# Kernel tuning notes

Measured on AMD Instinct MI355X. Metric: run time of the kernel, lower is better.

## Reference

```python
import jax, jax.numpy as jnp
import numpy as np

N = 50000      # n_nodes
S = 16         # neighbors per node
D_IN = 256     # raw feature dim
PREP = 128     # prep_len
H = 2          # n_head
OUT = 64       # per-head spec output_dim (concat_node doubles it)
MP = 2         # n_mp (metapaths)
IN2 = 2 * OUT * H  # layer-2 input dim = 256


def setup_inputs() -> dict:
    key = jax.random.key(0)
    ks = jax.random.split(key, 7)
    feats = jax.random.normal(ks[0], (N, D_IN), jnp.float32)
    prep_W = jax.random.normal(ks[1], (D_IN, PREP), jnp.float32) * 0.05
    Wx1 = jax.random.normal(ks[2], (MP, H, PREP, OUT), jnp.float32) * 0.05
    Wn1 = jax.random.normal(ks[3], (MP, H, PREP, OUT), jnp.float32) * 0.05
    Wx2 = jax.random.normal(ks[4], (MP, H, IN2, OUT), jnp.float32) * 0.05
    Wn2 = jax.random.normal(ks[5], (MP, H, IN2, OUT), jnp.float32) * 0.05
    node_neigh = jax.random.randint(ks[6], (MP, N, S), 0, N, dtype=jnp.int32)
    return {"feats": feats, "prep_W": prep_W, "Wx1": Wx1, "Wn1": Wn1,
            "Wx2": Wx2, "Wn2": Wn2, "node_neigh": node_neigh}


def _agg_layer(x, neigh, Wx, Wn):
    # x: [N, d]; neigh: [N, S]; Wx, Wn: [H, d, OUT]
    # neighbor gather + mean (the chunk_edge = all_feats[node_neigh] path)
    agg = jnp.mean(x[neigh], axis=1)                  # [N, d]
    xh = jnp.einsum('nd,hdo->nho', x, Wx)             # [N, H, OUT]
    nh = jnp.einsum('nd,hdo->nho', agg, Wn)           # [N, H, OUT]
    h = jax.nn.relu(jnp.concatenate([xh, nh], -1))    # per-head concat_node
    return h.reshape(x.shape[0], -1)                  # heads concatenated


def reference(feats, prep_W, Wx1, Wn1, Wx2, Wn2, node_neigh):
    # feats[all_ids].detach() in the original -> stop_gradient
    feats = jax.lax.stop_gradient(feats)
    outs = []
    for mp in range(MP):
        h0 = feats @ prep_W                           # prep (dummy == layer-1 prep here)
        neigh = node_neigh[mp]
        h1 = _agg_layer(h0, neigh, Wx1[mp], Wn1[mp])  # [N, 256]
        h2 = _agg_layer(h1, neigh, Wx2[mp], Wn2[mp])  # [N, 256]
        outs.append(jnp.concatenate([h1, h2], axis=-1))  # skip-buffer concat
    return jnp.stack(outs, axis=0)                    # [MP, N, 512]
```

## Files before the change

### kernel.cpp

```cpp
#include <hip/hip_runtime.h>

#define NN 50000
#define SNEI 16
#define GB 782

typedef unsigned short ushort_t;
typedef unsigned int uint_t;
typedef unsigned long long u64;
typedef __attribute__((ext_vector_type(8))) short bhalf8;
typedef __attribute__((ext_vector_type(4))) float facc4;

__device__ __forceinline__ float b2f(uint_t u) {
    union { uint_t u; float f; } x; x.u = u << 16; return x.f;
}
__device__ __forceinline__ ushort_t f2b(float f) {
    union { float f; uint_t u; } x; x.f = f;
    return (ushort_t)((x.u + 0x7FFFu + ((x.u >> 16) & 1u)) >> 16);
}
__device__ __forceinline__ u64 pack4(float a, float b, float c, float d) {
    return (u64)f2b(a) | ((u64)f2b(b) << 16) | ((u64)f2b(c) << 32) | ((u64)f2b(d) << 48);
}

typedef const __attribute__((address_space(1))) void cglb_t;
typedef __attribute__((address_space(3))) void lds3_t;
__device__ __forceinline__ void gload16(const void* g, void* l) {
    __builtin_amdgcn_global_load_lds((cglb_t*)g, (lds3_t*)l, 16, 0, 0);
}

__global__ void permSetup(const float* __restrict__ prepW,
                          const float* __restrict__ Wx1, const float* __restrict__ Wn1,
                          const float* __restrict__ Wx2, const float* __restrict__ Wn2,
                          ushort_t* __restrict__ dst)
{
    int e = blockIdx.x * 256 + threadIdx.x;
    int q8 = e >> 3, j = e & 7;
    int layer = q8 >> 14;
    int qq = q8 & 16383;
    int mp = qq >> 13, isN = (qq >> 12) & 1, q = qq & 4095;
    int lane = q & 63, nf = (q >> 6) & 7, ks = q >> 9;
    int c = nf * 16 + (lane & 15);
    int k = ks * 32 + ((lane >> 4) << 3) + j;
    float v;
    if (layer == 0) {
        const float* W1 = (isN ? Wn1 : Wx1) + mp * 16384 + (c >> 6) * 8192 + (c & 63);
        const float* pw = prepW + (size_t)k * 128;
        float s0 = 0.f, s1 = 0.f;
#pragma unroll 4
        for (int p = 0; p < 128; p += 2) {
            s0 += pw[p]     * W1[(size_t)p * 64];
            s1 += pw[p + 1] * W1[(size_t)(p + 1) * 64];
        }
        v = s0 + s1;
    } else {
        const float* W2 = (isN ? Wn2 : Wx2) + mp * 32768 + (c >> 6) * 16384 + (size_t)k * 64 + (c & 63);
        v = *W2;
    }
    dst[(size_t)q8 * 8 + j] = f2b(v);
}

template<bool XF32, bool L1>
__global__ __launch_bounds__(256, 4)
void proj_gemm(const void* __restrict__ Xv, size_t xStr,
               const ushort_t* __restrict__ W, size_t wStr,
               float* __restrict__ out, size_t oStr,
               ushort_t* __restrict__ h1, size_t hStr,
               ushort_t* __restrict__ P, size_t PStr)
{
    __shared__ bhalf8 lds[2560];
    u64* l64 = (u64*)lds;
    const int tid = threadIdx.x;
    const int lane = tid & 63;
    const int wid = tid >> 6;
    const int wave_m = wid >> 1, wave_n = wid & 1;
    const int m0 = blockIdx.x * 64;
    const int mp = blockIdx.y;

    const ushort_t* wx = W + (size_t)mp * wStr;
    const ushort_t* wn = wx + 4096 * 8;
    const float*    Xf = (const float*)Xv    + (size_t)mp * xStr;
    const ushort_t* Xb = (const ushort_t*)Xv + (size_t)mp * xStr;
    float* outp = out + (size_t)mp * oStr;
    ushort_t* h1p = L1 ? (h1 + (size_t)mp * hStr) : nullptr;
    ushort_t* Pp  = P + (size_t)mp * PStr;

    facc4 acc[2][8];
    const facc4 z = {0.f, 0.f, 0.f, 0.f};
#pragma unroll
    for (int i = 0; i < 2; ++i)
#pragma unroll
        for (int j = 0; j < 8; ++j) acc[i][j] = z;

    for (int kt = 0; kt < 4; ++kt) {
        if constexpr (XF32) {
#pragma unroll
            for (int it = 0; it < 2; ++it) {
                int s = tid + it * 256;
                int fp = s >> 6, ls = s & 63;
                int mf = fp & 3, ksl = fp >> 2;
                int grow = m0 + mf * 16 + (ls & 15); if (grow > NN - 1) grow = NN - 1;
                const float* gp = Xf + (size_t)grow * 256 + kt * 64 + ksl * 32 + ((ls >> 4) << 3);
                float4 f0 = *(const float4*)gp, f1 = *(const float4*)(gp + 4);
                l64[s * 2]     = pack4(f0.x, f0.y, f0.z, f0.w);
                l64[s * 2 + 1] = pack4(f1.x, f1.y, f1.z, f1.w);
            }
        } else {
#pragma unroll
            for (int it = 0; it < 2; ++it) {
                int u = wid + it * 4;
                int mf = u & 3, ksl = u >> 2;
                int grow = m0 + mf * 16 + (lane & 15); if (grow > NN - 1) grow = NN - 1;
                const ushort_t* src = Xb + (size_t)grow * 256 + kt * 64 + ksl * 32 + ((lane >> 4) << 3);
                gload16(src, (char*)lds + (u * 64 + lane) * 16);
            }
        }
#pragma unroll
        for (int it = 0; it < 4; ++it) {
            int cb = (it * 4 + wid) * 64;
            gload16(wx + ((size_t)kt * 1024 + cb + lane) * 8,
                    (char*)lds + (512 + cb + lane) * 16);
            gload16(wn + ((size_t)kt * 1024 + cb + lane) * 8,
                    (char*)lds + (1536 + cb + lane) * 16);
        }
        __syncthreads();
        const int wB = wave_n ? 1536 : 512;
#pragma unroll
        for (int ksl = 0; ksl < 2; ++ksl) {
            bhalf8 a0 = lds[(ksl * 4 + wave_m * 2 + 0) * 64 + lane];
            bhalf8 a1 = lds[(ksl * 4 + wave_m * 2 + 1) * 64 + lane];
#pragma unroll
            for (int nf = 0; nf < 8; ++nf) {
                bhalf8 b = lds[wB + (ksl * 8 + nf) * 64 + lane];
                acc[0][nf] = __builtin_amdgcn_mfma_f32_16x16x32_bf16(a0, b, acc[0][nf], 0, 0, 0);
                acc[1][nf] = __builtin_amdgcn_mfma_f32_16x16x32_bf16(a1, b, acc[1][nf], 0, 0, 0);
            }
        }
        __syncthreads();
    }
    const int cl = lane & 15, rg = lane >> 4;
    const int obase = L1 ? 0 : 256;
#pragma unroll
    for (int mf2 = 0; mf2 < 2; ++mf2) {
        int rowb = m0 + (wave_m * 2 + mf2) * 16 + rg * 4;
#pragma unroll
        for (int nf = 0; nf < 8; ++nf) {
            int cpr = nf * 16 + cl;
            int icol = (cpr >> 6) * 128 + (cpr & 63);
            facc4 v = acc[mf2][nf];
#pragma unroll
            for (int rr = 0; rr < 4; ++rr) {
                int row = rowb + rr;
                if (row < NN) {
                    if (wave_n == 0) {
                        float f = fmaxf(v[rr], 0.0f);
                        outp[(size_t)row * 512 + obase + icol] = f;
                        if constexpr (L1)
                            h1p[(size_t)row * 256 + icol] = f2b(f);
                    } else {
                        Pp[(size_t)(cpr >> 5) * (NN * 32) + (size_t)row * 32 + (cpr & 31)] = f2b(v[rr]);
                    }
                }
            }
        }
    }
}

template<bool L1>
__global__ __launch_bounds__(256)
void gatherS(const ushort_t* __restrict__ P, size_t PStr,
             const int* __restrict__ nb, size_t nStr,
             float* __restrict__ out, size_t oStr,
             ushort_t* __restrict__ h1, size_t hStr)
{
    const int slice = blockIdx.y;
    const int mp = blockIdx.z;
    const ushort_t* Pp = P + (size_t)mp * PStr + (size_t)slice * (NN * 32);
    const int* nbp = nb + (size_t)mp * nStr;
    float* outp = out + (size_t)mp * oStr;

    __shared__ int nls[1024];
    const int nodeBase = blockIdx.x * 64;
    {
        int i4 = nodeBase * 4 + threadIdx.x;
        int mx = NN * 4 - 1;
        if (i4 > mx) i4 = mx;
        ((int4*)nls)[threadIdx.x] = ((const int4*)nbp)[i4];
    }
    __syncthreads();

    const int nl = threadIdx.x >> 2, q = threadIdx.x & 3;
    const int node = nodeBase + nl;
    if (node >= NN) return;
    const int* nr = nls + nl * SNEI;
    float a0=0.f,a1=0.f,a2=0.f,a3=0.f,a4=0.f,a5=0.f,a6=0.f,a7=0.f;
#pragma unroll
    for (int s = 0; s < SNEI; ++s) {
        uint4 v = *(const uint4*)(Pp + (size_t)nr[s] * 32 + q * 8);
        a0 += b2f(v.x & 0xFFFFu); a1 += b2f(v.x >> 16);
        a2 += b2f(v.y & 0xFFFFu); a3 += b2f(v.y >> 16);
        a4 += b2f(v.z & 0xFFFFu); a5 += b2f(v.z >> 16);
        a6 += b2f(v.w & 0xFFFFu); a7 += b2f(v.w >> 16);
    }
    const float M = 0.0625f;
    float r0 = fmaxf(a0*M, 0.f), r1 = fmaxf(a1*M, 0.f);
    float r2 = fmaxf(a2*M, 0.f), r3 = fmaxf(a3*M, 0.f);
    float r4 = fmaxf(a4*M, 0.f), r5 = fmaxf(a5*M, 0.f);
    float r6 = fmaxf(a6*M, 0.f), r7 = fmaxf(a7*M, 0.f);
    const int head = slice >> 1;
    const int coff = head * 128 + 64 + (slice & 1) * 32 + q * 8;
    const int obase = L1 ? 0 : 256;
    float* o = outp + (size_t)node * 512 + obase + coff;
    *(float4*)o       = make_float4(r0, r1, r2, r3);
    *(float4*)(o + 4) = make_float4(r4, r5, r6, r7);
    if constexpr (L1) {
        ushort_t* hp = h1 + (size_t)mp * hStr + (size_t)node * 256 + coff;
        *(u64*)hp       = pack4(r0, r1, r2, r3);
        *(u64*)(hp + 4) = pack4(r4, r5, r6, r7);
    }
}

extern "C" void kernel_launch(void* const* d_in, const int* in_sizes, int n_in,
                              void* d_out, int out_size, void* d_ws, size_t ws_size,
                              hipStream_t stream)
{
    const float* feats  = (const float*)d_in[0];
    const float* prepWp = (const float*)d_in[1];
    const float* Wx1    = (const float*)d_in[2];
    const float* Wn1    = (const float*)d_in[3];
    const float* Wx2    = (const float*)d_in[4];
    const float* Wn2    = (const float*)d_in[5];
    const int*   neigh  = (const int*)d_in[6];
    float* out = (float*)d_out;
    ushort_t* ws = (ushort_t*)d_ws;

    const size_t permElems = 262144;
    const size_t needBatched = permElems * 2
        + 2 * ((size_t)NN * 128 * 2 + (size_t)NN * 256 * 2);
    const bool batched = ws_size >= needBatched;
    const int nmp = batched ? 2 : 1;

    ushort_t* perm = ws;
    ushort_t* P    = ws + permElems;
    ushort_t* h1   = P + (size_t)nmp * NN * 128;

    permSetup<<<1024, 256, 0, stream>>>(prepWp, Wx1, Wn1, Wx2, Wn2, perm);

    const size_t PStr = batched ? (size_t)NN * 128 : 0;
    const size_t hStr = batched ? (size_t)NN * 256 : 0;
    const size_t oStr = batched ? (size_t)NN * 512 : 0;
    const size_t nStr = batched ? (size_t)NN * SNEI : 0;
    const size_t wStr = batched ? (size_t)8192 * 8 : 0;
    const int passes = batched ? 1 : 2;

    for (int p = 0; p < passes; ++p) {
        const ushort_t* w1 = perm + (size_t)p * 8192 * 8;
        const ushort_t* w2 = perm + (size_t)(16384 + p * 8192) * 8;
        float* outp = out + (size_t)p * NN * 512;
        const int* nbp = neigh + (size_t)p * NN * SNEI;
        dim3 gp(GB, nmp), gg(GB, 4, nmp);

        proj_gemm<true, true><<<gp, 256, 0, stream>>>(
            feats, 0, w1, wStr, outp, oStr, h1, hStr, P, PStr);
        gatherS<true><<<gg, 256, 0, stream>>>(
            P, PStr, nbp, nStr, outp, oStr, h1, hStr);
        proj_gemm<false, false><<<gp, 256, 0, stream>>>(
            h1, hStr, w2, wStr, outp, oStr, nullptr, 0, P, PStr);
        gatherS<false><<<gg, 256, 0, stream>>>(
            P, PStr, nbp, nStr, outp, oStr, nullptr, 0);
    }
}
```

Before: 195.1 us.

## Drop bf16 h1 buffer, read layer-2 input from fp32 output, reorder gather grid

Removes the separate bf16 copy of h1. The layer-2 GEMM now reads the fp32 layer-1 half of the output tensor directly, converting it to bf16 while staging into LDS, which saves one buffer write. Output and P stores become nontemporal. The gather grid is flattened so that all slices and metapaths of a node block are adjacent, which should improve locality of the neighbor-index loads. In exchange, layer 2 reads 4-byte instead of 2-byte activations through a strided fp32 path rather than direct global-to-LDS loads, and the nontemporal hint may push P out of cache right before the gather kernel reads it.

```diff
diff --git a/kernel.cpp b/kernel.cpp
--- a/kernel.cpp
+++ b/kernel.cpp
@@ -9,6 +9,7 @@
 typedef unsigned long long u64;
 typedef __attribute__((ext_vector_type(8))) short bhalf8;
 typedef __attribute__((ext_vector_type(4))) float facc4;
+typedef __attribute__((ext_vector_type(4))) float f32x4;
 
 __device__ __forceinline__ float b2f(uint_t u) {
     union { uint_t u; float f; } x; x.u = u << 16; return x.f;
@@ -58,13 +59,11 @@
     dst[(size_t)q8 * 8 + j] = f2b(v);
 }
 
-template<bool XF32, bool L1>
 __global__ __launch_bounds__(256, 4)
-void proj_gemm(const void* __restrict__ Xv, size_t xStr,
-               const ushort_t* __restrict__ W, size_t wStr,
-               float* __restrict__ out, size_t oStr,
-               ushort_t* __restrict__ h1, size_t hStr,
-               ushort_t* __restrict__ P, size_t PStr)
+void proj_gemm(const float* __restrict__ X, int xPitch, size_t xMpStr,
+               const ushort_t* __restrict__ W, size_t wMpStr,
+               float* __restrict__ out, size_t oMpStr, int obase,
+               ushort_t* __restrict__ P, size_t PMpStr)
 {
     __shared__ bhalf8 lds[2560];
     u64* l64 = (u64*)lds;
@@ -75,13 +74,11 @@
     const int m0 = blockIdx.x * 64;
     const int mp = blockIdx.y;
 
-    const ushort_t* wx = W + (size_t)mp * wStr;
+    const float* Xp = X + (size_t)mp * xMpStr;
+    const ushort_t* wx = W + (size_t)mp * wMpStr;
     const ushort_t* wn = wx + 4096 * 8;
-    const float*    Xf = (const float*)Xv    + (size_t)mp * xStr;
-    const ushort_t* Xb = (const ushort_t*)Xv + (size_t)mp * xStr;
-    float* outp = out + (size_t)mp * oStr;
-    ushort_t* h1p = L1 ? (h1 + (size_t)mp * hStr) : nullptr;
-    ushort_t* Pp  = P + (size_t)mp * PStr;
+    float* outp = out + (size_t)mp * oMpStr;
+    ushort_t* Pp = P + (size_t)mp * PMpStr;
 
     facc4 acc[2][8];
     const facc4 z = {0.f, 0.f, 0.f, 0.f};
@@ -91,27 +88,16 @@
         for (int j = 0; j < 8; ++j) acc[i][j] = z;
 
     for (int kt = 0; kt < 4; ++kt) {
-        if constexpr (XF32) {
-#pragma unroll
-            for (int it = 0; it < 2; ++it) {
-                int s = tid + it * 256;
-                int fp = s >> 6, ls = s & 63;
-                int mf = fp & 3, ksl = fp >> 2;
-                int grow = m0 + mf * 16 + (ls & 15); if (grow > NN - 1) grow = NN - 1;
-                const float* gp = Xf + (size_t)grow * 256 + kt * 64 + ksl * 32 + ((ls >> 4) << 3);
-                float4 f0 = *(const float4*)gp, f1 = *(const float4*)(gp + 4);
-                l64[s * 2]     = pack4(f0.x, f0.y, f0.z, f0.w);
-                l64[s * 2 + 1] = pack4(f1.x, f1.y, f1.z, f1.w);
-            }
-        } else {
-#pragma unroll
-            for (int it = 0; it < 2; ++it) {
-                int u = wid + it * 4;
-                int mf = u & 3, ksl = u >> 2;
-                int grow = m0 + mf * 16 + (lane & 15); if (grow > NN - 1) grow = NN - 1;
-                const ushort_t* src = Xb + (size_t)grow * 256 + kt * 64 + ksl * 32 + ((lane >> 4) << 3);
-                gload16(src, (char*)lds + (u * 64 + lane) * 16);
-            }
+#pragma unroll
+        for (int it = 0; it < 2; ++it) {
+            int s = tid + it * 256;
+            int fp = s >> 6, ls = s & 63;
+            int mf = fp & 3, ksl = fp >> 2;
+            int row = m0 + mf * 16 + (ls & 15); if (row > NN - 1) row = NN - 1;
+            const float* gp = Xp + (size_t)row * xPitch + kt * 64 + ksl * 32 + ((ls >> 4) << 3);
+            float4 f0 = *(const float4*)gp, f1 = *(const float4*)(gp + 4);
+            l64[s * 2]     = pack4(f0.x, f0.y, f0.z, f0.w);
+            l64[s * 2 + 1] = pack4(f1.x, f1.y, f1.z, f1.w);
         }
 #pragma unroll
         for (int it = 0; it < 4; ++it) {
@@ -137,7 +123,6 @@
         __syncthreads();
     }
     const int cl = lane & 15, rg = lane >> 4;
-    const int obase = L1 ? 0 : 256;
 #pragma unroll
     for (int mf2 = 0; mf2 < 2; ++mf2) {
         int rowb = m0 + (wave_m * 2 + mf2) * 16 + rg * 4;
@@ -152,11 +137,10 @@
                 if (row < NN) {
                     if (wave_n == 0) {
                         float f = fmaxf(v[rr], 0.0f);
-                        outp[(size_t)row * 512 + obase + icol] = f;
-                        if constexpr (L1)
-                            h1p[(size_t)row * 256 + icol] = f2b(f);
+                        __builtin_nontemporal_store(f, &outp[(size_t)row * 512 + obase + icol]);
                     } else {
-                        Pp[(size_t)(cpr >> 5) * (NN * 32) + (size_t)row * 32 + (cpr & 31)] = f2b(v[rr]);
+                        __builtin_nontemporal_store(f2b(v[rr]),
+                            &Pp[(size_t)(cpr >> 5) * (NN * 32) + (size_t)row * 32 + (cpr & 31)]);
                     }
                 }
             }
@@ -164,21 +148,22 @@
     }
 }
 
-template<bool L1>
 __global__ __launch_bounds__(256)
-void gatherS(const ushort_t* __restrict__ P, size_t PStr,
-             const int* __restrict__ nb, size_t nStr,
-             float* __restrict__ out, size_t oStr,
-             ushort_t* __restrict__ h1, size_t hStr)
-{
-    const int slice = blockIdx.y;
-    const int mp = blockIdx.z;
-    const ushort_t* Pp = P + (size_t)mp * PStr + (size_t)slice * (NN * 32);
-    const int* nbp = nb + (size_t)mp * nStr;
-    float* outp = out + (size_t)mp * oStr;
+void gatherS(const ushort_t* __restrict__ P, size_t PMpStr,
+             const int* __restrict__ nb, size_t nMpStr,
+             float* __restrict__ out, size_t oMpStr,
+             int obase, int shift)
+{
+    const int b = blockIdx.x;
+    const int pair = b & ((1 << shift) - 1);
+    const int slice = pair & 3, mp = pair >> 2;
+    const int nodeBase = (b >> shift) * 64;
+
+    const ushort_t* Pp = P + (size_t)mp * PMpStr + (size_t)slice * (NN * 32);
+    const int* nbp = nb + (size_t)mp * nMpStr;
+    float* outp = out + (size_t)mp * oMpStr;
 
     __shared__ int nls[1024];
-    const int nodeBase = blockIdx.x * 64;
     {
         int i4 = nodeBase * 4 + threadIdx.x;
         int mx = NN * 4 - 1;
@@ -201,21 +186,12 @@
         a6 += b2f(v.w & 0xFFFFu); a7 += b2f(v.w >> 16);
     }
     const float M = 0.0625f;
-    float r0 = fmaxf(a0*M, 0.f), r1 = fmaxf(a1*M, 0.f);
-    float r2 = fmaxf(a2*M, 0.f), r3 = fmaxf(a3*M, 0.f);
-    float r4 = fmaxf(a4*M, 0.f), r5 = fmaxf(a5*M, 0.f);
-    float r6 = fmaxf(a6*M, 0.f), r7 = fmaxf(a7*M, 0.f);
-    const int head = slice >> 1;
-    const int coff = head * 128 + 64 + (slice & 1) * 32 + q * 8;
-    const int obase = L1 ? 0 : 256;
+    f32x4 r0 = { fmaxf(a0*M, 0.f), fmaxf(a1*M, 0.f), fmaxf(a2*M, 0.f), fmaxf(a3*M, 0.f) };
+    f32x4 r1 = { fmaxf(a4*M, 0.f), fmaxf(a5*M, 0.f), fmaxf(a6*M, 0.f), fmaxf(a7*M, 0.f) };
+    const int coff = (slice >> 1) * 128 + 64 + (slice & 1) * 32 + q * 8;
     float* o = outp + (size_t)node * 512 + obase + coff;
-    *(float4*)o       = make_float4(r0, r1, r2, r3);
-    *(float4*)(o + 4) = make_float4(r4, r5, r6, r7);
-    if constexpr (L1) {
-        ushort_t* hp = h1 + (size_t)mp * hStr + (size_t)node * 256 + coff;
-        *(u64*)hp       = pack4(r0, r1, r2, r3);
-        *(u64*)(hp + 4) = pack4(r4, r5, r6, r7);
-    }
+    __builtin_nontemporal_store(r0, (f32x4*)o);
+    __builtin_nontemporal_store(r1, (f32x4*)(o + 4));
 }
 
 extern "C" void kernel_launch(void* const* d_in, const int* in_sizes, int n_in,
@@ -233,22 +209,20 @@
     ushort_t* ws = (ushort_t*)d_ws;
 
     const size_t permElems = 262144;
-    const size_t needBatched = permElems * 2
-        + 2 * ((size_t)NN * 128 * 2 + (size_t)NN * 256 * 2);
+    const size_t needBatched = (permElems + 2 * (size_t)NN * 128) * 2;
     const bool batched = ws_size >= needBatched;
     const int nmp = batched ? 2 : 1;
 
     ushort_t* perm = ws;
     ushort_t* P    = ws + permElems;
-    ushort_t* h1   = P + (size_t)nmp * NN * 128;
 
     permSetup<<<1024, 256, 0, stream>>>(prepWp, Wx1, Wn1, Wx2, Wn2, perm);
 
     const size_t PStr = batched ? (size_t)NN * 128 : 0;
-    const size_t hStr = batched ? (size_t)NN * 256 : 0;
     const size_t oStr = batched ? (size_t)NN * 512 : 0;
     const size_t nStr = batched ? (size_t)NN * SNEI : 0;
     const size_t wStr = batched ? (size_t)8192 * 8 : 0;
+    const int shift = batched ? 3 : 2;
     const int passes = batched ? 1 : 2;
 
     for (int p = 0; p < passes; ++p) {
@@ -256,15 +230,15 @@
         const ushort_t* w2 = perm + (size_t)(16384 + p * 8192) * 8;
         float* outp = out + (size_t)p * NN * 512;
         const int* nbp = neigh + (size_t)p * NN * SNEI;
-        dim3 gp(GB, nmp), gg(GB, 4, nmp);
-
-        proj_gemm<true, true><<<gp, 256, 0, stream>>>(
-            feats, 0, w1, wStr, outp, oStr, h1, hStr, P, PStr);
-        gatherS<true><<<gg, 256, 0, stream>>>(
-            P, PStr, nbp, nStr, outp, oStr, h1, hStr);
-        proj_gemm<false, false><<<gp, 256, 0, stream>>>(
-            h1, hStr, w2, wStr, outp, oStr, nullptr, 0, P, PStr);
-        gatherS<false><<<gg, 256, 0, stream>>>(
-            P, PStr, nbp, nStr, outp, oStr, nullptr, 0);
-    }
-}
+        dim3 gp(GB, nmp);
+        const int gg = GB << shift;
+
+        proj_gemm<<<gp, 256, 0, stream>>>(feats, 256, 0,
+                                          w1, wStr, outp, oStr, 0, P, PStr);
+        gatherS<<<gg, 256, 0, stream>>>(P, PStr, nbp, nStr, outp, oStr, 0, shift);
+
+        proj_gemm<<<gp, 256, 0, stream>>>(outp, 512, oStr,
+                                          w2, wStr, outp, oStr, 256, P, PStr);
+        gatherS<<<gg, 256, 0, stream>>>(P, PStr, nbp, nStr, outp, oStr, 256, shift);
+    }
+}
```

Measured after the change: 203.4 us. +4.2%, slower.
